# Kernel optimization log

Measured on AMD Instinct MI355X. Metric: run time of the kernel, lower is better.

## Reference

```python
import jax, jax.numpy as jnp
import numpy as np

CODEBOOK_SIZE = 4096
DIM = 64


def setup_inputs() -> dict:
    key = jax.random.key(0)
    kx, ke = jax.random.split(key)
    x = jax.random.normal(kx, (8, 4096, DIM), dtype=jnp.float32)
    embed = jax.random.normal(ke, (CODEBOOK_SIZE, DIM), dtype=jnp.float32)  # codebook [K, d]
    return {"x": x, "embed": embed}


def reference(x, embed):
    # Eval-mode forward of EuclideanCodebook (svq_temp=None -> argmax).
    shape = x.shape
    flatten = x.reshape(-1, shape[-1])            # [N, d]
    embed_sq = jnp.sum(embed * embed, axis=-1)    # [K]
    # dist = 2 * x @ embed.T - ||embed||^2  (negative squared distance up to a const in x)
    dist = 2.0 * jnp.matmul(flatten, embed.T) - embed_sq[None, :]  # [N, K]
    embed_ind = jnp.argmax(dist, axis=-1)         # [N]
    embed_ind = embed_ind.reshape(shape[:-1])     # [...]
    quantize = embed[embed_ind]                   # gather -> [..., d]
    return (quantize, embed_ind)
```

## Files before the change

kernel.cpp:

```cpp
#include <hip/hip_runtime.h>
#include <math.h>

#define N_ROWS 32768
#define K_CODES 4096
#define DIM 64
#define SPLITS 2
#define TILES_TOTAL (K_CODES / 32)
#define TILES_PER_SPLIT (TILES_TOTAL / SPLITS)
#define QUANT_ELEMS (N_ROWS * DIM)

typedef _Float16 half8 __attribute__((ext_vector_type(8)));
typedef float floatx16 __attribute__((ext_vector_type(16)));

__global__ void embed_sq_kernel(const float* __restrict__ embed,
                                float* __restrict__ sq) {
    int k = blockIdx.x * blockDim.x + threadIdx.x;
    if (k >= K_CODES) return;
    const float4* e4 = reinterpret_cast<const float4*>(embed + (size_t)k * DIM);
    float a0 = 0.f, a1 = 0.f, a2 = 0.f, a3 = 0.f;
#pragma unroll
    for (int i = 0; i < DIM / 4; ++i) {
        float4 v = e4[i];
        a0 = fmaf(v.x, v.x, a0);
        a1 = fmaf(v.y, v.y, a1);
        a2 = fmaf(v.z, v.z, a2);
        a3 = fmaf(v.w, v.w, a3);
    }
    sq[k] = (a0 + a1) + (a2 + a3);
}

__global__ void frag_convert_kernel(const float* __restrict__ embed,
                                    half8* __restrict__ ehi,
                                    half8* __restrict__ elo) {
    int t = blockIdx.x * blockDim.x + threadIdx.x;
    if (t >= TILES_TOTAL * 4 * 64) return;
    int l = t & 63;
    int s = (t >> 6) & 3;
    int c = t >> 8;
    int code = c * 32 + (l & 31);
    int koff = (l >> 5) * 8 + 16 * s;
    const float* src = embed + (size_t)code * DIM + koff;
    half8 h, lo;
#pragma unroll
    for (int j = 0; j < 8; ++j) {
        float v = src[j];
        _Float16 hi = (_Float16)v;
        h[j] = hi;
        lo[j] = (_Float16)(v - (float)hi);
    }
    ehi[t] = h;
    elo[t] = lo;
}

__global__ __launch_bounds__(256, 2) void fused_dist_argmax32(
    const float* __restrict__ x, const float* __restrict__ sq,
    const half8* __restrict__ ehi, const half8* __restrict__ elo,
    float* __restrict__ pbest, int* __restrict__ pidx) {
    const int lane = threadIdx.x & 63;
    const int wave = threadIdx.x >> 6;
    const int col = lane & 31;
    const int half_ = lane >> 5;
    const int row_base = blockIdx.x * 128 + wave * 32;
    const int split = blockIdx.y;
    const int c0 = split * TILES_PER_SPLIT;

    half8 ah[4], al[4];
    {
        const float* xs = x + (size_t)(row_base + col) * DIM + half_ * 8;
#pragma unroll
        for (int s = 0; s < 4; ++s) {
            half8 h, lo;
#pragma unroll
            for (int j = 0; j < 8; ++j) {
                float v = 2.0f * xs[16 * s + j];
                _Float16 hi = (_Float16)v;
                h[j] = hi;
                lo[j] = (_Float16)(v - (float)hi);
            }
            ah[s] = h;
            al[s] = lo;
        }
    }

    float best[16];
    int bidx[16];
#pragma unroll
    for (int r = 0; r < 16; ++r) {
        best[r] = -INFINITY;
        bidx[r] = 0;
    }

    const half8* ph = ehi + (size_t)c0 * 256 + lane;
    const half8* pl = elo + (size_t)c0 * 256 + lane;
    const float* psq = sq + c0 * 32 + col;

    for (int c = 0; c < TILES_PER_SPLIT; ++c) {
        half8 bh0 = ph[0], bh1 = ph[64], bh2 = ph[128], bh3 = ph[192];
        half8 bl0 = pl[0], bl1 = pl[64], bl2 = pl[128], bl3 = pl[192];
        float nsq = -psq[0];
        ph += 256;
        pl += 256;
        psq += 32;

        floatx16 acc;
#pragma unroll
        for (int r = 0; r < 16; ++r) acc[r] = nsq;
        acc = __builtin_amdgcn_mfma_f32_32x32x16_f16(ah[0], bh0, acc, 0, 0, 0);
        acc = __builtin_amdgcn_mfma_f32_32x32x16_f16(ah[1], bh1, acc, 0, 0, 0);
        acc = __builtin_amdgcn_mfma_f32_32x32x16_f16(ah[2], bh2, acc, 0, 0, 0);
        acc = __builtin_amdgcn_mfma_f32_32x32x16_f16(ah[3], bh3, acc, 0, 0, 0);
        acc = __builtin_amdgcn_mfma_f32_32x32x16_f16(al[0], bh0, acc, 0, 0, 0);
        acc = __builtin_amdgcn_mfma_f32_32x32x16_f16(al[1], bh1, acc, 0, 0, 0);
        acc = __builtin_amdgcn_mfma_f32_32x32x16_f16(al[2], bh2, acc, 0, 0, 0);
        acc = __builtin_amdgcn_mfma_f32_32x32x16_f16(al[3], bh3, acc, 0, 0, 0);
        acc = __builtin_amdgcn_mfma_f32_32x32x16_f16(ah[0], bl0, acc, 0, 0, 0);
        acc = __builtin_amdgcn_mfma_f32_32x32x16_f16(ah[1], bl1, acc, 0, 0, 0);
        acc = __builtin_amdgcn_mfma_f32_32x32x16_f16(ah[2], bl2, acc, 0, 0, 0);
        acc = __builtin_amdgcn_mfma_f32_32x32x16_f16(ah[3], bl3, acc, 0, 0, 0);

        const int cidx = (c0 + c) * 32 + col;
#pragma unroll
        for (int r = 0; r < 16; ++r) {
            if (acc[r] > best[r]) {
                best[r] = acc[r];
                bidx[r] = cidx;
            }
        }
    }

#pragma unroll
    for (int r = 0; r < 16; ++r) {
        float bv = best[r];
        int bi = bidx[r];
#pragma unroll
        for (int d = 1; d < 32; d <<= 1) {
            float ov = __shfl_xor(bv, d);
            int oi = __shfl_xor(bi, d);
            if (ov > bv || (ov == bv && oi < bi)) {
                bv = ov;
                bi = oi;
            }
        }
        if (col == 0) {
            const int row = row_base + (r & 3) + 8 * (r >> 2) + 4 * half_;
            pbest[(size_t)split * N_ROWS + row] = bv;
            pidx[(size_t)split * N_ROWS + row] = bi;
        }
    }
}

__global__ void combine_kernel(const float* __restrict__ pbest,
                               const int* __restrict__ pidx,
                               const float* __restrict__ embed,
                               float* __restrict__ out) {
    const int t = blockIdx.x * blockDim.x + threadIdx.x;
    const int row = t >> 4;
    const int q = t & 15;
    if (row >= N_ROWS) return;

    float best = -INFINITY;
    int bi = 0;
#pragma unroll
    for (int s = 0; s < SPLITS; ++s) {
        float b = pbest[(size_t)s * N_ROWS + row];
        int i = pidx[(size_t)s * N_ROWS + row];
        if (b > best) {
            best = b;
            bi = i;
        }
    }

    const float4* e4 = reinterpret_cast<const float4*>(embed);
    float4 v = e4[(size_t)bi * (DIM / 4) + q];
    reinterpret_cast<float4*>(out)[(size_t)row * (DIM / 4) + q] = v;
    if (q == 0) {
        out[(size_t)QUANT_ELEMS + row] = (float)bi;
    }
}

extern "C" void kernel_launch(void* const* d_in, const int* in_sizes, int n_in,
                              void* d_out, int out_size, void* d_ws,
                              size_t ws_size, hipStream_t stream) {
    const float* x = (const float*)d_in[0];
    const float* embed = (const float*)d_in[1];
    float* out = (float*)d_out;

    char* ws = (char*)d_ws;
    float* sq = (float*)ws;
    half8* ehi = (half8*)(ws + 16384);
    half8* elo = (half8*)(ws + 16384 + 524288);
    float* pbest = (float*)(ws + 16384 + 2 * 524288);
    int* pidx = (int*)(ws + 16384 + 2 * 524288 + SPLITS * N_ROWS * 4);

    embed_sq_kernel<<<(K_CODES + 255) / 256, 256, 0, stream>>>(embed, sq);

    frag_convert_kernel<<<(TILES_TOTAL * 4 * 64 + 255) / 256, 256, 0,
                          stream>>>(embed, ehi, elo);

    dim3 grid(N_ROWS / 128, SPLITS);
    fused_dist_argmax32<<<grid, 256, 0, stream>>>(x, sq, ehi, elo, pbest,
                                                  pidx);

    const int combine_threads = N_ROWS * (DIM / 4);
    combine_kernel<<<(combine_threads + 255) / 256, 256, 0, stream>>>(
        pbest, pidx, embed, out);
}
```

Before: 144.5 us.

## Stage codebook tiles via global_load_lds, fuse prep kernels, raise splits and occupancy

Merges the squared-norm and fp16 hi/lo fragment conversion kernels into one prep kernel that reduces norms through shared memory. The main kernel now loads each codebook tile cooperatively into LDS with global_load_lds, so four waves share one copy instead of each wave reading it from global memory separately. It also doubles the code splits to 4 and raises the launch-bounds occupancy hint to 4. The cost is two block barriers per tile with no double buffering, so load latency is exposed at each iteration, plus more partial results for the combine step to merge.

```diff
diff --git a/kernel.cpp b/kernel.cpp
--- a/kernel.cpp
+++ b/kernel.cpp
@@ -4,7 +4,7 @@
 #define N_ROWS 32768
 #define K_CODES 4096
 #define DIM 64
-#define SPLITS 2
+#define SPLITS 4
 #define TILES_TOTAL (K_CODES / 32)
 #define TILES_PER_SPLIT (TILES_TOTAL / SPLITS)
 #define QUANT_ELEMS (N_ROWS * DIM)
@@ -12,52 +12,55 @@
 typedef _Float16 half8 __attribute__((ext_vector_type(8)));
 typedef float floatx16 __attribute__((ext_vector_type(16)));
 
-__global__ void embed_sq_kernel(const float* __restrict__ embed,
-                                float* __restrict__ sq) {
-    int k = blockIdx.x * blockDim.x + threadIdx.x;
-    if (k >= K_CODES) return;
-    const float4* e4 = reinterpret_cast<const float4*>(embed + (size_t)k * DIM);
-    float a0 = 0.f, a1 = 0.f, a2 = 0.f, a3 = 0.f;
-#pragma unroll
-    for (int i = 0; i < DIM / 4; ++i) {
-        float4 v = e4[i];
-        a0 = fmaf(v.x, v.x, a0);
-        a1 = fmaf(v.y, v.y, a1);
-        a2 = fmaf(v.z, v.z, a2);
-        a3 = fmaf(v.w, v.w, a3);
-    }
-    sq[k] = (a0 + a1) + (a2 + a3);
-}
-
-__global__ void frag_convert_kernel(const float* __restrict__ embed,
-                                    half8* __restrict__ ehi,
-                                    half8* __restrict__ elo) {
-    int t = blockIdx.x * blockDim.x + threadIdx.x;
-    if (t >= TILES_TOTAL * 4 * 64) return;
-    int l = t & 63;
-    int s = (t >> 6) & 3;
-    int c = t >> 8;
-    int code = c * 32 + (l & 31);
-    int koff = (l >> 5) * 8 + 16 * s;
+__device__ __forceinline__ void gld16(const void* g, void* l) {
+    __builtin_amdgcn_global_load_lds(
+        (const __attribute__((address_space(1))) unsigned int*)g,
+        (__attribute__((address_space(3))) unsigned int*)l, 16, 0, 0);
+}
+
+__global__ void prep_kernel(const float* __restrict__ embed,
+                            float* __restrict__ sq, half8* __restrict__ ehi,
+                            half8* __restrict__ elo) {
+    __shared__ float part[256];
+    const int tid = threadIdx.x;
+    const int t = blockIdx.x * 256 + tid;
+    const int l = t & 63;
+    const int s = (t >> 6) & 3;
+    const int c = blockIdx.x;
+    const int col = l & 31;
+    const int code = c * 32 + col;
+    const int koff = (l >> 5) * 8 + 16 * s;
     const float* src = embed + (size_t)code * DIM + koff;
     half8 h, lo;
+    float ss = 0.f;
 #pragma unroll
     for (int j = 0; j < 8; ++j) {
         float v = src[j];
+        ss = fmaf(v, v, ss);
         _Float16 hi = (_Float16)v;
         h[j] = hi;
         lo[j] = (_Float16)(v - (float)hi);
     }
     ehi[t] = h;
     elo[t] = lo;
-}
-
-__global__ __launch_bounds__(256, 2) void fused_dist_argmax32(
+    part[tid] = ss;
+    __syncthreads();
+    if (tid < 32) {
+        float a = 0.f;
+#pragma unroll
+        for (int q = 0; q < 8; ++q) a += part[tid + 32 * (q & 1) + 64 * (q >> 1)];
+        sq[c * 32 + tid] = a;
+    }
+}
+
+__global__ __launch_bounds__(256, 4) void fused_dist_argmax32(
     const float* __restrict__ x, const float* __restrict__ sq,
     const half8* __restrict__ ehi, const half8* __restrict__ elo,
     float* __restrict__ pbest, int* __restrict__ pidx) {
-    const int lane = threadIdx.x & 63;
-    const int wave = threadIdx.x >> 6;
+    __shared__ char lbuf[8192];
+    const int tid = threadIdx.x;
+    const int lane = tid & 63;
+    const int wave = tid >> 6;
     const int col = lane & 31;
     const int half_ = lane >> 5;
     const int row_base = blockIdx.x * 128 + wave * 32;
@@ -90,33 +93,43 @@
         bidx[r] = 0;
     }
 
-    const half8* ph = ehi + (size_t)c0 * 256 + lane;
-    const half8* pl = elo + (size_t)c0 * 256 + lane;
+    const char* gh = (const char*)(ehi + (size_t)c0 * 256);
+    const char* gl = (const char*)(elo + (size_t)c0 * 256);
     const float* psq = sq + c0 * 32 + col;
+    const half8* lh = (const half8*)lbuf;
+    const half8* ll = (const half8*)(lbuf + 4096);
 
     for (int c = 0; c < TILES_PER_SPLIT; ++c) {
-        half8 bh0 = ph[0], bh1 = ph[64], bh2 = ph[128], bh3 = ph[192];
-        half8 bl0 = pl[0], bl1 = pl[64], bl2 = pl[128], bl3 = pl[192];
-        float nsq = -psq[0];
-        ph += 256;
-        pl += 256;
-        psq += 32;
+        gld16(gh + (size_t)c * 4096 + (size_t)tid * 16, lbuf + tid * 16);
+        gld16(gl + (size_t)c * 4096 + (size_t)tid * 16, lbuf + 4096 + tid * 16);
+        float nsq = -psq[(size_t)c * 32];
+        __syncthreads();
 
         floatx16 acc;
 #pragma unroll
         for (int r = 0; r < 16; ++r) acc[r] = nsq;
-        acc = __builtin_amdgcn_mfma_f32_32x32x16_f16(ah[0], bh0, acc, 0, 0, 0);
-        acc = __builtin_amdgcn_mfma_f32_32x32x16_f16(ah[1], bh1, acc, 0, 0, 0);
-        acc = __builtin_amdgcn_mfma_f32_32x32x16_f16(ah[2], bh2, acc, 0, 0, 0);
-        acc = __builtin_amdgcn_mfma_f32_32x32x16_f16(ah[3], bh3, acc, 0, 0, 0);
-        acc = __builtin_amdgcn_mfma_f32_32x32x16_f16(al[0], bh0, acc, 0, 0, 0);
-        acc = __builtin_amdgcn_mfma_f32_32x32x16_f16(al[1], bh1, acc, 0, 0, 0);
-        acc = __builtin_amdgcn_mfma_f32_32x32x16_f16(al[2], bh2, acc, 0, 0, 0);
-        acc = __builtin_amdgcn_mfma_f32_32x32x16_f16(al[3], bh3, acc, 0, 0, 0);
-        acc = __builtin_amdgcn_mfma_f32_32x32x16_f16(ah[0], bl0, acc, 0, 0, 0);
-        acc = __builtin_amdgcn_mfma_f32_32x32x16_f16(ah[1], bl1, acc, 0, 0, 0);
-        acc = __builtin_amdgcn_mfma_f32_32x32x16_f16(ah[2], bl2, acc, 0, 0, 0);
-        acc = __builtin_amdgcn_mfma_f32_32x32x16_f16(ah[3], bl3, acc, 0, 0, 0);
+        half8 b;
+        b = lh[lane];
+        acc = __builtin_amdgcn_mfma_f32_32x32x16_f16(ah[0], b, acc, 0, 0, 0);
+        acc = __builtin_amdgcn_mfma_f32_32x32x16_f16(al[0], b, acc, 0, 0, 0);
+        b = lh[64 + lane];
+        acc = __builtin_amdgcn_mfma_f32_32x32x16_f16(ah[1], b, acc, 0, 0, 0);
+        acc = __builtin_amdgcn_mfma_f32_32x32x16_f16(al[1], b, acc, 0, 0, 0);
+        b = lh[128 + lane];
+        acc = __builtin_amdgcn_mfma_f32_32x32x16_f16(ah[2], b, acc, 0, 0, 0);
+        acc = __builtin_amdgcn_mfma_f32_32x32x16_f16(al[2], b, acc, 0, 0, 0);
+        b = lh[192 + lane];
+        acc = __builtin_amdgcn_mfma_f32_32x32x16_f16(ah[3], b, acc, 0, 0, 0);
+        acc = __builtin_amdgcn_mfma_f32_32x32x16_f16(al[3], b, acc, 0, 0, 0);
+        b = ll[lane];
+        acc = __builtin_amdgcn_mfma_f32_32x32x16_f16(ah[0], b, acc, 0, 0, 0);
+        b = ll[64 + lane];
+        acc = __builtin_amdgcn_mfma_f32_32x32x16_f16(ah[1], b, acc, 0, 0, 0);
+        b = ll[128 + lane];
+        acc = __builtin_amdgcn_mfma_f32_32x32x16_f16(ah[2], b, acc, 0, 0, 0);
+        b = ll[192 + lane];
+        acc = __builtin_amdgcn_mfma_f32_32x32x16_f16(ah[3], b, acc, 0, 0, 0);
+        __syncthreads();
 
         const int cidx = (c0 + c) * 32 + col;
 #pragma unroll
@@ -192,10 +205,7 @@
     float* pbest = (float*)(ws + 16384 + 2 * 524288);
     int* pidx = (int*)(ws + 16384 + 2 * 524288 + SPLITS * N_ROWS * 4);
 
-    embed_sq_kernel<<<(K_CODES + 255) / 256, 256, 0, stream>>>(embed, sq);
-
-    frag_convert_kernel<<<(TILES_TOTAL * 4 * 64 + 255) / 256, 256, 0,
-                          stream>>>(embed, ehi, elo);
+    prep_kernel<<<TILES_TOTAL, 256, 0, stream>>>(embed, sq, ehi, elo);
 
     dim3 grid(N_ROWS / 128, SPLITS);
     fused_dist_argmax32<<<grid, 256, 0, stream>>>(x, sq, ehi, elo, pbest,
```

After: 122.6 us. 15.1% less time.
